# Kernel tuning notes

Measured on AMD Instinct MI355X. Metric: run time of the kernel, lower is better.

The kernel has to match this reference:

```python
import jax, jax.numpy as jnp
import numpy as np

NUM_SIN = 8
HIDDEN = 64
COND = 128
OUT = 4
SQRT2 = 1.4142135623730951


def coords_to_sinusoidals(coords):
    # coords: [..., 2]; per-frequency blocks of 4: [sin_x, sin_y, cos_x, cos_y]
    freqs = 2.0 ** jnp.arange(NUM_SIN, dtype=coords.dtype)  # mult freq_type, multiplier=2
    ang = coords[..., None, :] * freqs[:, None]              # [..., 8, 2]
    emb = jnp.concatenate([jnp.sin(ang), jnp.cos(ang)], axis=-1)  # [..., 8, 4]
    return emb.reshape(coords.shape[:-1] + (2 * 2 * NUM_SIN,))


def equal_linear(x, w, b, lrelu):
    scale = 1.0 / np.sqrt(w.shape[1])  # lr_mul = 1
    y = x @ (w * scale).T + b
    if lrelu:
        y = jax.nn.leaky_relu(y, 0.2) * SQRT2  # fused_lrelu
    return y


def setup_inputs() -> dict:
    key = jax.random.key(0)
    ks = jax.random.split(key, 8)
    coords = jax.random.normal(ks[0], (8, 256, 256, 2), dtype=jnp.float32)
    c = jax.random.normal(ks[1], (8, COND), dtype=jnp.float32)
    freq_unlock = jax.random.uniform(ks[2], (1,), dtype=jnp.float32)
    in1 = 2 * 2 * NUM_SIN + COND  # 160
    in2 = HIDDEN + COND           # 192
    w1 = jax.random.normal(ks[3], (HIDDEN, in1), dtype=jnp.float32)
    w2 = jax.random.normal(ks[4], (HIDDEN, in2), dtype=jnp.float32)
    w3 = jax.random.normal(ks[5], (HIDDEN, in2), dtype=jnp.float32)
    w4 = jax.random.normal(ks[6], (OUT, in2), dtype=jnp.float32)
    b1 = jnp.zeros((HIDDEN,), jnp.float32)
    b2 = jnp.zeros((HIDDEN,), jnp.float32)
    b3 = jnp.zeros((HIDDEN,), jnp.float32)
    b4 = jnp.zeros((OUT,), jnp.float32)
    return {"coords": coords, "c": c, "freq_unlock": freq_unlock,
            "w1": w1, "b1": b1, "w2": w2, "b2": b2,
            "w3": w3, "b3": b3, "w4": w4, "b4": b4}


def reference(coords, c, freq_unlock, w1, b1, w2, b2, w3, b3, w4, b4):
    B, H, W, _ = coords.shape
    emb = coords_to_sinusoidals(coords / 10.0)  # [B,H,W,32]
    # progressive frequency masking
    limits = jnp.arange(1, NUM_SIN + 1, dtype=coords.dtype) / (NUM_SIN + 1)
    weights = jnp.clip((freq_unlock[0] - limits) * (NUM_SIN + 1), 0.0, 1.0)  # [8]
    emb = emb * jnp.repeat(weights, 4)  # blocks of 4 per frequency
    x = emb.reshape(B * H * W, -1)
    cf = jnp.broadcast_to(c[:, None, None, :], (B, H, W, COND)).reshape(B * H * W, COND)
    h = equal_linear(jnp.concatenate([x, cf], -1), w1, b1, True)
    h = equal_linear(jnp.concatenate([h, cf], -1), w2, b2, True)
    h = equal_linear(jnp.concatenate([h, cf], -1), w3, b3, True)
    h = equal_linear(jnp.concatenate([h, cf], -1), w4, b4, False)
    out = h.reshape(B, H, W, OUT)
    # radius masking
    radius = jnp.sqrt(jnp.sum(coords ** 2, axis=-1, keepdims=True))
    out = out * (1.0 - jnp.tanh(jax.nn.relu(radius - 1.0)))
    return out
```

## Files before the change

kernel.cpp:

```cpp
#include <hip/hip_runtime.h>
#include <math.h>


typedef _Float16 half2v __attribute__((ext_vector_type(2)));
typedef __fp16   fp16x2 __attribute__((ext_vector_type(2)));
typedef _Float16 half4v __attribute__((ext_vector_type(4)));
typedef _Float16 half8  __attribute__((ext_vector_type(8)));
typedef float f32x16 __attribute__((ext_vector_type(16)));

#define SCALE1 0.0790569415042094833f
#define SCALE2 0.0721687836487032206f
#define SQRT2F 1.41421356237309515f

#define FE_L1 0
#define FE_L2 256
#define FE_L3 768
#define FE_L4 1280
#define FE_TOT 1536
#define OFF_CB1 6144
#define OFF_CB2 6656
#define OFF_CB3 7168
#define OFF_CB4 7680

__global__ __launch_bounds__(256) void prep_kernel(
    const float* __restrict__ c, const float* __restrict__ fu,
    const float* __restrict__ w1, const float* __restrict__ b1,
    const float* __restrict__ w2, const float* __restrict__ b2,
    const float* __restrict__ w3, const float* __restrict__ b3,
    const float* __restrict__ w4, const float* __restrict__ b4,
    float* __restrict__ ws)
{
  int t = blockIdx.x * 256 + threadIdx.x;
  if (t < 12288) {
    _Float16* fr = (_Float16*)ws;
    int e, Ktm;
    const float* w; float scale; int stride; bool perm;
    if (t < 2048)       { e = t;         Ktm = 2; w = w1; scale = SCALE1;          stride = 160; perm = false; }
    else if (t < 6144)  { e = t - 2048;  Ktm = 4; w = w2; scale = SCALE2 * SQRT2F; stride = 192; perm = true;  }
    else if (t < 10240) { e = t - 6144;  Ktm = 4; w = w3; scale = SCALE2 * SQRT2F; stride = 192; perm = true;  }
    else                { e = t - 10240; Ktm = 4; w = w4; scale = SCALE2 * SQRT2F; stride = 192; perm = true;  }
    int til  = e >> 9;
    int lane = (e >> 3) & 63;
    int r    = e & 7;
    int q    = lane >> 5;
    int mt = til / Ktm, kt = til - mt * Ktm;
    int j = 32 * mt + (lane & 31);
    int k;
    if (perm) {
      k = 32 * (kt >> 1) + 16 * (kt & 1) + 8 * (r >> 2) + 4 * q + (r & 3);
    } else {
      k = 16 * kt + 8 * q + r;
    }
    float val;
    if (t < 2048) {
      float mw = (fu[0] - (float)((k >> 2) + 1) * (1.0f / 9.0f)) * 9.0f;
      mw = fminf(fmaxf(mw, 0.0f), 1.0f);
      val = w[j * stride + k] * scale * mw;
    } else if (t >= 10240) {
      val = (j < 4) ? w[j * stride + k] * scale : 0.0f;
    } else {
      val = w[j * stride + k] * scale;
    }
    fr[t] = (_Float16)val;
  } else if (t < 12288 + 2048) {
    int u = t - 12288;
    int grp = u >> 9;
    const float* wr; float bias; float scale; int outoff;
    int b, j;
    if (grp < 3) {
      b = (u & 511) >> 6; j = u & 63;
      if (grp == 0)      { wr = w1 + j * 160 + 32; bias = b1[j]; scale = SCALE1; outoff = OFF_CB1 + b * 64 + j; }
      else if (grp == 1) { wr = w2 + j * 192 + 64; bias = b2[j]; scale = SCALE2; outoff = OFF_CB2 + b * 64 + j; }
      else               { wr = w3 + j * 192 + 64; bias = b3[j]; scale = SCALE2; outoff = OFF_CB3 + b * 64 + j; }
    } else {
      int u2 = u - 1536;
      if (u2 >= 32) return;
      b = u2 >> 2; j = u2 & 3;
      wr = w4 + j * 192 + 64; bias = b4[j]; scale = SCALE2; outoff = OFF_CB4 + b * 4 + j;
    }
    const float4* wv = (const float4*)wr;
    const float4* cv = (const float4*)(c + b * 128);
    float4 s = make_float4(0.f, 0.f, 0.f, 0.f);
    #pragma unroll
    for (int k = 0; k < 32; ++k) {
      float4 a = wv[k], d = cv[k];
      s.x = fmaf(a.x, d.x, s.x);
      s.y = fmaf(a.y, d.y, s.y);
      s.z = fmaf(a.z, d.z, s.z);
      s.w = fmaf(a.w, d.w, s.w);
    }
    float dot = (s.x + s.y) + (s.z + s.w);
    ws[outoff] = fmaf(scale, dot, bias);
  }
}

__global__ __launch_bounds__(256, 4) void decoder_main(
    const float2* __restrict__ coords, const float* __restrict__ ws,
    float4* __restrict__ out)
{
  __shared__ __align__(16) _Float16 sfr_raw[FE_TOT * 8];
  half8* __restrict__ sfr = (half8*)sfr_raw;

  const int tid  = threadIdx.x;
  const int lane = tid & 63;
  const int wave = tid >> 6;
  const int base = blockIdx.x * 256 + wave * 64;
  const int b    = base >> 16;
  const int col  = lane & 31;
  const bool hi  = lane >= 32;
  const int q4   = hi ? 4 : 0;

  const half8* __restrict__ gfr = (const half8*)ws;
  #pragma unroll
  for (int i = 0; i < 6; ++i) {
    const int e = tid + 256 * i;
    sfr[e] = gfr[e];
  }

  const float* __restrict__ cb1 = ws + OFF_CB1 + b * 64;
  const float* __restrict__ cb2 = ws + OFF_CB2 + b * 64;
  const float* __restrict__ cb3 = ws + OFF_CB3 + b * 64;
  const float* __restrict__ cb4 = ws + OFF_CB4 + b * 4;

  const int p0 = base + col, p1 = base + 32 + col;
  const float2 cc0 = coords[p0];
  const float2 cc1 = coords[p1];

  half8 bf[2][2];
  {
    const float qm = hi ? 0.4f : 0.1f;
    auto chain = [](float a, float* s, float* c) {
      float s0 = __sinf(a), c0 = __cosf(a);
      s[0] = s0; c[0] = c0;
      float s1 = 2.f * s0 * c0, c1 = (c0 - s0) * (c0 + s0);
      s[1] = s1; c[1] = c1;
      float s2 = 2.f * s1 * c1, c2 = (c1 - s1) * (c1 + s1);
      float s3 = 2.f * s2 * c2, c3 = (c2 - s2) * (c2 + s2);
      float s4 = 2.f * s3 * c3, c4 = (c3 - s3) * (c3 + s3);
      s[2] = s4; c[2] = c4;
      float s5 = 2.f * s4 * c4, c5 = (c4 - s4) * (c4 + s4);
      s[3] = s5; c[3] = c5;
    };
    #pragma unroll
    for (int nt = 0; nt < 2; ++nt) {
      const float2 cc = nt ? cc1 : cc0;
      float sx[4], cx[4], sy[4], cy[4];
      chain(cc.x * qm, sx, cx);
      chain(cc.y * qm, sy, cy);
      #pragma unroll
      for (int kt = 0; kt < 2; ++kt) {
        const int i0 = 2 * kt, i1 = 2 * kt + 1;
        half2v p0v = __builtin_bit_cast(half2v, __builtin_amdgcn_cvt_pkrtz(sx[i0], sy[i0]));
        half2v p1v = __builtin_bit_cast(half2v, __builtin_amdgcn_cvt_pkrtz(cx[i0], cy[i0]));
        half2v p2v = __builtin_bit_cast(half2v, __builtin_amdgcn_cvt_pkrtz(sx[i1], sy[i1]));
        half2v p3v = __builtin_bit_cast(half2v, __builtin_amdgcn_cvt_pkrtz(cx[i1], cy[i1]));
        half4v q0 = __builtin_shufflevector(p0v, p1v, 0, 1, 2, 3);
        half4v q1 = __builtin_shufflevector(p2v, p3v, 0, 1, 2, 3);
        bf[nt][kt] = __builtin_shufflevector(q0, q1, 0, 1, 2, 3, 4, 5, 6, 7);
      }
    }
  }

  __syncthreads();

  f32x16 acc[2][2];
  half8 nbf[2][4];

  auto transition = [&]() {
    #pragma unroll
    for (int mt = 0; mt < 2; ++mt)
      #pragma unroll
      for (int nt = 0; nt < 2; ++nt) {
        #pragma unroll
        for (int h = 0; h < 2; ++h) {
          half2v pp[4];
          #pragma unroll
          for (int p = 0; p < 4; ++p) {
            fp16x2 t = __builtin_amdgcn_cvt_pkrtz(acc[mt][nt][8 * h + 2 * p],
                                                  acc[mt][nt][8 * h + 2 * p + 1]);
            pp[p] = __builtin_bit_cast(half2v, t);
          }
          half4v q0 = __builtin_shufflevector(pp[0], pp[1], 0, 1, 2, 3);
          half4v q1 = __builtin_shufflevector(pp[2], pp[3], 0, 1, 2, 3);
          half8 f = __builtin_shufflevector(q0, q1, 0, 1, 2, 3, 4, 5, 6, 7);
          half8 f2 = f * (_Float16)0.2f;
          nbf[nt][2 * mt + h] = __builtin_elementwise_max(f, f2);
        }
      }
  };

  auto init_acc = [&](const float* __restrict__ cb) {
    #pragma unroll
    for (int mt = 0; mt < 2; ++mt)
      #pragma unroll
      for (int g = 0; g < 4; ++g) {
        const float4 f = *(const float4*)(cb + 32 * mt + 8 * g + q4);
        #pragma unroll
        for (int nt = 0; nt < 2; ++nt) {
          acc[mt][nt][4 * g + 0] = f.x;
          acc[mt][nt][4 * g + 1] = f.y;
          acc[mt][nt][4 * g + 2] = f.z;
          acc[mt][nt][4 * g + 3] = f.w;
        }
      }
  };

  init_acc(cb1);
  #pragma unroll
  for (int kt = 0; kt < 2; ++kt) {
    half8 a0 = sfr[FE_L1 + (0 * 2 + kt) * 64 + lane];
    half8 a1 = sfr[FE_L1 + (1 * 2 + kt) * 64 + lane];
    acc[0][0] = __builtin_amdgcn_mfma_f32_32x32x16_f16(a0, bf[0][kt], acc[0][0], 0, 0, 0);
    acc[0][1] = __builtin_amdgcn_mfma_f32_32x32x16_f16(a0, bf[1][kt], acc[0][1], 0, 0, 0);
    acc[1][0] = __builtin_amdgcn_mfma_f32_32x32x16_f16(a1, bf[0][kt], acc[1][0], 0, 0, 0);
    acc[1][1] = __builtin_amdgcn_mfma_f32_32x32x16_f16(a1, bf[1][kt], acc[1][1], 0, 0, 0);
  }
  transition();

  #pragma unroll
  for (int layer = 0; layer < 2; ++layer) {
    const int fe = layer == 0 ? FE_L2 : FE_L3;
    init_acc(layer == 0 ? cb2 : cb3);
    #pragma unroll
    for (int kt = 0; kt < 4; ++kt) {
      half8 a0 = sfr[fe + (0 * 4 + kt) * 64 + lane];
      half8 a1 = sfr[fe + (1 * 4 + kt) * 64 + lane];
      acc[0][0] = __builtin_amdgcn_mfma_f32_32x32x16_f16(a0, nbf[0][kt], acc[0][0], 0, 0, 0);
      acc[0][1] = __builtin_amdgcn_mfma_f32_32x32x16_f16(a0, nbf[1][kt], acc[0][1], 0, 0, 0);
      acc[1][0] = __builtin_amdgcn_mfma_f32_32x32x16_f16(a1, nbf[0][kt], acc[1][0], 0, 0, 0);
      acc[1][1] = __builtin_amdgcn_mfma_f32_32x32x16_f16(a1, nbf[1][kt], acc[1][1], 0, 0, 0);
    }
    transition();
  }

  f32x16 acc4[2];
  {
    const float c0 = cb4[0], c1 = cb4[1], c2 = cb4[2], c3 = cb4[3];
    #pragma unroll
    for (int r = 0; r < 16; ++r) { acc4[0][r] = 0.f; acc4[1][r] = 0.f; }
    if (!hi) {
      acc4[0][0] = c0; acc4[0][1] = c1; acc4[0][2] = c2; acc4[0][3] = c3;
      acc4[1][0] = c0; acc4[1][1] = c1; acc4[1][2] = c2; acc4[1][3] = c3;
    }
  }
  #pragma unroll
  for (int kt = 0; kt < 4; ++kt) {
    half8 a0 = sfr[FE_L4 + kt * 64 + lane];
    acc4[0] = __builtin_amdgcn_mfma_f32_32x32x16_f16(a0, nbf[0][kt], acc4[0], 0, 0, 0);
    acc4[1] = __builtin_amdgcn_mfma_f32_32x32x16_f16(a0, nbf[1][kt], acc4[1], 0, 0, 0);
  }

  if (!hi) {
    #pragma unroll
    for (int nt = 0; nt < 2; ++nt) {
      const float2 cc = nt ? cc1 : cc0;
      const float rad = sqrtf(cc.x * cc.x + cc.y * cc.y);
      const float tt = fmaxf(rad - 1.0f, 0.0f);
      const float m = 2.0f / (__expf(2.0f * tt) + 1.0f);
      out[nt ? p1 : p0] = make_float4(acc4[nt][0] * m, acc4[nt][1] * m,
                                      acc4[nt][2] * m, acc4[nt][3] * m);
    }
  }
}

extern "C" void kernel_launch(void* const* d_in, const int* in_sizes, int n_in,
                              void* d_out, int out_size, void* d_ws, size_t ws_size,
                              hipStream_t stream) {
  const float* coords = (const float*)d_in[0];
  const float* c      = (const float*)d_in[1];
  const float* fu     = (const float*)d_in[2];
  const float* w1     = (const float*)d_in[3];
  const float* b1     = (const float*)d_in[4];
  const float* w2     = (const float*)d_in[5];
  const float* b2     = (const float*)d_in[6];
  const float* w3     = (const float*)d_in[7];
  const float* b3     = (const float*)d_in[8];
  const float* w4     = (const float*)d_in[9];
  const float* b4     = (const float*)d_in[10];
  float* ws  = (float*)d_ws;
  float* out = (float*)d_out;

  int npix = in_sizes[0] / 2;

  prep_kernel<<<56, 256, 0, stream>>>(c, fu, w1, b1, w2, b2, w3, b3, w4, b4, ws);
  decoder_main<<<npix / 256, 256, 0, stream>>>(
      (const float2*)coords, ws, (float4*)out);
}
```

Baseline: 97.80 us.

## Process two pixel tiles per block and stage weights via direct global-to-LDS loads

Each block now handles 512 pixels in two sequential passes, so the 24KB fp16 weight fragment load into LDS is amortized over twice the work and only one barrier is needed. Weights and per-batch bias vectors are loaded with global_load_lds (bypassing VGPRs), and biases now come from LDS instead of global memory. Halving the grid reduces the number of blocks and may reduce parallelism or tail balance, and the wave-3-only bias load relies on the single barrier for visibility.

```diff
diff --git a/kernel.cpp b/kernel.cpp
--- a/kernel.cpp
+++ b/kernel.cpp
@@ -99,13 +99,13 @@
     float4* __restrict__ out)
 {
   __shared__ __align__(16) _Float16 sfr_raw[FE_TOT * 8];
+  __shared__ __align__(16) float scb[256];
   half8* __restrict__ sfr = (half8*)sfr_raw;
 
   const int tid  = threadIdx.x;
   const int lane = tid & 63;
   const int wave = tid >> 6;
-  const int base = blockIdx.x * 256 + wave * 64;
-  const int b    = base >> 16;
+  const int b    = blockIdx.x >> 7;
   const int col  = lane & 31;
   const bool hi  = lane >= 32;
   const int q4   = hi ? 4 : 0;
@@ -113,55 +113,31 @@
   const half8* __restrict__ gfr = (const half8*)ws;
   #pragma unroll
   for (int i = 0; i < 6; ++i) {
-    const int e = tid + 256 * i;
-    sfr[e] = gfr[e];
+    const int e0 = wave * 64 + 256 * i;
+    __builtin_amdgcn_global_load_lds(
+        (const __attribute__((address_space(1))) void*)(gfr + e0 + lane),
+        (__attribute__((address_space(3))) void*)(sfr_raw + e0 * 8),
+        16, 0, 0);
   }
-
-  const float* __restrict__ cb1 = ws + OFF_CB1 + b * 64;
-  const float* __restrict__ cb2 = ws + OFF_CB2 + b * 64;
-  const float* __restrict__ cb3 = ws + OFF_CB3 + b * 64;
-  const float* __restrict__ cb4 = ws + OFF_CB4 + b * 4;
-
-  const int p0 = base + col, p1 = base + 32 + col;
-  const float2 cc0 = coords[p0];
-  const float2 cc1 = coords[p1];
-
-  half8 bf[2][2];
-  {
-    const float qm = hi ? 0.4f : 0.1f;
-    auto chain = [](float a, float* s, float* c) {
-      float s0 = __sinf(a), c0 = __cosf(a);
-      s[0] = s0; c[0] = c0;
-      float s1 = 2.f * s0 * c0, c1 = (c0 - s0) * (c0 + s0);
-      s[1] = s1; c[1] = c1;
-      float s2 = 2.f * s1 * c1, c2 = (c1 - s1) * (c1 + s1);
-      float s3 = 2.f * s2 * c2, c3 = (c2 - s2) * (c2 + s2);
-      float s4 = 2.f * s3 * c3, c4 = (c3 - s3) * (c3 + s3);
-      s[2] = s4; c[2] = c4;
-      float s5 = 2.f * s4 * c4, c5 = (c4 - s4) * (c4 + s4);
-      s[3] = s5; c[3] = c5;
-    };
-    #pragma unroll
-    for (int nt = 0; nt < 2; ++nt) {
-      const float2 cc = nt ? cc1 : cc0;
-      float sx[4], cx[4], sy[4], cy[4];
-      chain(cc.x * qm, sx, cx);
-      chain(cc.y * qm, sy, cy);
-      #pragma unroll
-      for (int kt = 0; kt < 2; ++kt) {
-        const int i0 = 2 * kt, i1 = 2 * kt + 1;
-        half2v p0v = __builtin_bit_cast(half2v, __builtin_amdgcn_cvt_pkrtz(sx[i0], sy[i0]));
-        half2v p1v = __builtin_bit_cast(half2v, __builtin_amdgcn_cvt_pkrtz(cx[i0], cy[i0]));
-        half2v p2v = __builtin_bit_cast(half2v, __builtin_amdgcn_cvt_pkrtz(sx[i1], sy[i1]));
-        half2v p3v = __builtin_bit_cast(half2v, __builtin_amdgcn_cvt_pkrtz(cx[i1], cy[i1]));
-        half4v q0 = __builtin_shufflevector(p0v, p1v, 0, 1, 2, 3);
-        half4v q1 = __builtin_shufflevector(p2v, p3v, 0, 1, 2, 3);
-        bf[nt][kt] = __builtin_shufflevector(q0, q1, 0, 1, 2, 3, 4, 5, 6, 7);
-      }
-    }
+  if (wave == 3) {
+    __builtin_amdgcn_global_load_lds(
+        (const __attribute__((address_space(1))) void*)(ws + OFF_CB1 + b * 64 + lane),
+        (__attribute__((address_space(3))) void*)(scb + 0), 4, 0, 0);
+    __builtin_amdgcn_global_load_lds(
+        (const __attribute__((address_space(1))) void*)(ws + OFF_CB2 + b * 64 + lane),
+        (__attribute__((address_space(3))) void*)(scb + 64), 4, 0, 0);
+    __builtin_amdgcn_global_load_lds(
+        (const __attribute__((address_space(1))) void*)(ws + OFF_CB3 + b * 64 + lane),
+        (__attribute__((address_space(3))) void*)(scb + 128), 4, 0, 0);
+    __builtin_amdgcn_global_load_lds(
+        (const __attribute__((address_space(1))) void*)(ws + OFF_CB4 + b * 4 + lane),
+        (__attribute__((address_space(3))) void*)(scb + 192), 4, 0, 0);
   }
 
-  __syncthreads();
+  const float2* __restrict__ cptr = coords + blockIdx.x * 512 + wave * 64;
+  float2 cc[2][2];
+  cc[0][0] = cptr[col];       cc[0][1] = cptr[32 + col];
+  cc[1][0] = cptr[256 + col]; cc[1][1] = cptr[288 + col];
 
   f32x16 acc[2][2];
   half8 nbf[2][4];
@@ -205,60 +181,101 @@
       }
   };
 
-  init_acc(cb1);
   #pragma unroll
-  for (int kt = 0; kt < 2; ++kt) {
-    half8 a0 = sfr[FE_L1 + (0 * 2 + kt) * 64 + lane];
-    half8 a1 = sfr[FE_L1 + (1 * 2 + kt) * 64 + lane];
-    acc[0][0] = __builtin_amdgcn_mfma_f32_32x32x16_f16(a0, bf[0][kt], acc[0][0], 0, 0, 0);
-    acc[0][1] = __builtin_amdgcn_mfma_f32_32x32x16_f16(a0, bf[1][kt], acc[0][1], 0, 0, 0);
-    acc[1][0] = __builtin_amdgcn_mfma_f32_32x32x16_f16(a1, bf[0][kt], acc[1][0], 0, 0, 0);
-    acc[1][1] = __builtin_amdgcn_mfma_f32_32x32x16_f16(a1, bf[1][kt], acc[1][1], 0, 0, 0);
-  }
-  transition();
-
-  #pragma unroll
-  for (int layer = 0; layer < 2; ++layer) {
-    const int fe = layer == 0 ? FE_L2 : FE_L3;
-    init_acc(layer == 0 ? cb2 : cb3);
+  for (int t = 0; t < 2; ++t) {
+    half8 bf[2][2];
+    {
+      const float qm = hi ? 0.4f : 0.1f;
+      auto chain = [](float a, float* s, float* c) {
+        float s0 = __sinf(a), c0 = __cosf(a);
+        s[0] = s0; c[0] = c0;
+        float s1 = 2.f * s0 * c0, c1 = (c0 - s0) * (c0 + s0);
+        s[1] = s1; c[1] = c1;
+        float s2 = 2.f * s1 * c1, c2 = (c1 - s1) * (c1 + s1);
+        float s3 = 2.f * s2 * c2, c3 = (c2 - s2) * (c2 + s2);
+        float s4 = 2.f * s3 * c3, c4 = (c3 - s3) * (c3 + s3);
+        s[2] = s4; c[2] = c4;
+        float s5 = 2.f * s4 * c4, c5 = (c4 - s4) * (c4 + s4);
+        s[3] = s5; c[3] = c5;
+      };
+      #pragma unroll
+      for (int nt = 0; nt < 2; ++nt) {
+        const float2 ccv = cc[t][nt];
+        float sx[4], cx[4], sy[4], cy[4];
+        chain(ccv.x * qm, sx, cx);
+        chain(ccv.y * qm, sy, cy);
+        #pragma unroll
+        for (int kt = 0; kt < 2; ++kt) {
+          const int i0 = 2 * kt, i1 = 2 * kt + 1;
+          half2v p0v = __builtin_bit_cast(half2v, __builtin_amdgcn_cvt_pkrtz(sx[i0], sy[i0]));
+          half2v p1v = __builtin_bit_cast(half2v, __builtin_amdgcn_cvt_pkrtz(cx[i0], cy[i0]));
+          half2v p2v = __builtin_bit_cast(half2v, __builtin_amdgcn_cvt_pkrtz(sx[i1], sy[i1]));
+          half2v p3v = __builtin_bit_cast(half2v, __builtin_amdgcn_cvt_pkrtz(cx[i1], cy[i1]));
+          half4v q0 = __builtin_shufflevector(p0v, p1v, 0, 1, 2, 3);
+          half4v q1 = __builtin_shufflevector(p2v, p3v, 0, 1, 2, 3);
+          bf[nt][kt] = __builtin_shufflevector(q0, q1, 0, 1, 2, 3, 4, 5, 6, 7);
+        }
+      }
+    }
+
+    if (t == 0) __syncthreads();
+
+    init_acc(scb + 0);
+    #pragma unroll
+    for (int kt = 0; kt < 2; ++kt) {
+      half8 a0 = sfr[FE_L1 + (0 * 2 + kt) * 64 + lane];
+      half8 a1 = sfr[FE_L1 + (1 * 2 + kt) * 64 + lane];
+      acc[0][0] = __builtin_amdgcn_mfma_f32_32x32x16_f16(a0, bf[0][kt], acc[0][0], 0, 0, 0);
+      acc[0][1] = __builtin_amdgcn_mfma_f32_32x32x16_f16(a0, bf[1][kt], acc[0][1], 0, 0, 0);
+      acc[1][0] = __builtin_amdgcn_mfma_f32_32x32x16_f16(a1, bf[0][kt], acc[1][0], 0, 0, 0);
+      acc[1][1] = __builtin_amdgcn_mfma_f32_32x32x16_f16(a1, bf[1][kt], acc[1][1], 0, 0, 0);
+    }
+    transition();
+
+    #pragma unroll
+    for (int layer = 0; layer < 2; ++layer) {
+      const int fe = layer == 0 ? FE_L2 : FE_L3;
+      init_acc(layer == 0 ? scb + 64 : scb + 128);
+      #pragma unroll
+      for (int kt = 0; kt < 4; ++kt) {
+        half8 a0 = sfr[fe + (0 * 4 + kt) * 64 + lane];
+        half8 a1 = sfr[fe + (1 * 4 + kt) * 64 + lane];
+        acc[0][0] = __builtin_amdgcn_mfma_f32_32x32x16_f16(a0, nbf[0][kt], acc[0][0], 0, 0, 0);
+        acc[0][1] = __builtin_amdgcn_mfma_f32_32x32x16_f16(a0, nbf[1][kt], acc[0][1], 0, 0, 0);
+        acc[1][0] = __builtin_amdgcn_mfma_f32_32x32x16_f16(a1, nbf[0][kt], acc[1][0], 0, 0, 0);
+        acc[1][1] = __builtin_amdgcn_mfma_f32_32x32x16_f16(a1, nbf[1][kt], acc[1][1], 0, 0, 0);
+      }
+      transition();
+    }
+
+    f32x16 acc4[2];
+    {
+      const float c0 = scb[192], c1 = scb[193], c2 = scb[194], c3 = scb[195];
+      #pragma unroll
+      for (int r = 0; r < 16; ++r) { acc4[0][r] = 0.f; acc4[1][r] = 0.f; }
+      if (!hi) {
+        acc4[0][0] = c0; acc4[0][1] = c1; acc4[0][2] = c2; acc4[0][3] = c3;
+        acc4[1][0] = c0; acc4[1][1] = c1; acc4[1][2] = c2; acc4[1][3] = c3;
+      }
+    }
     #pragma unroll
     for (int kt = 0; kt < 4; ++kt) {
-      half8 a0 = sfr[fe + (0 * 4 + kt) * 64 + lane];
-      half8 a1 = sfr[fe + (1 * 4 + kt) * 64 + lane];
-      acc[0][0] = __builtin_amdgcn_mfma_f32_32x32x16_f16(a0, nbf[0][kt], acc[0][0], 0, 0, 0);
-      acc[0][1] = __builtin_amdgcn_mfma_f32_32x32x16_f16(a0, nbf[1][kt], acc[0][1], 0, 0, 0);
-      acc[1][0] = __builtin_amdgcn_mfma_f32_32x32x16_f16(a1, nbf[0][kt], acc[1][0], 0, 0, 0);
-      acc[1][1] = __builtin_amdgcn_mfma_f32_32x32x16_f16(a1, nbf[1][kt], acc[1][1], 0, 0, 0);
-    }
-    transition();
-  }
-
-  f32x16 acc4[2];
-  {
-    const float c0 = cb4[0], c1 = cb4[1], c2 = cb4[2], c3 = cb4[3];
-    #pragma unroll
-    for (int r = 0; r < 16; ++r) { acc4[0][r] = 0.f; acc4[1][r] = 0.f; }
+      half8 a0 = sfr[FE_L4 + kt * 64 + lane];
+      acc4[0] = __builtin_amdgcn_mfma_f32_32x32x16_f16(a0, nbf[0][kt], acc4[0], 0, 0, 0);
+      acc4[1] = __builtin_amdgcn_mfma_f32_32x32x16_f16(a0, nbf[1][kt], acc4[1], 0, 0, 0);
+    }
+
     if (!hi) {
-      acc4[0][0] = c0; acc4[0][1] = c1; acc4[0][2] = c2; acc4[0][3] = c3;
-      acc4[1][0] = c0; acc4[1][1] = c1; acc4[1][2] = c2; acc4[1][3] = c3;
-    }
-  }
-  #pragma unroll
-  for (int kt = 0; kt < 4; ++kt) {
-    half8 a0 = sfr[FE_L4 + kt * 64 + lane];
-    acc4[0] = __builtin_amdgcn_mfma_f32_32x32x16_f16(a0, nbf[0][kt], acc4[0], 0, 0, 0);
-    acc4[1] = __builtin_amdgcn_mfma_f32_32x32x16_f16(a0, nbf[1][kt], acc4[1], 0, 0, 0);
-  }
-
-  if (!hi) {
-    #pragma unroll
-    for (int nt = 0; nt < 2; ++nt) {
-      const float2 cc = nt ? cc1 : cc0;
-      const float rad = sqrtf(cc.x * cc.x + cc.y * cc.y);
-      const float tt = fmaxf(rad - 1.0f, 0.0f);
-      const float m = 2.0f / (__expf(2.0f * tt) + 1.0f);
-      out[nt ? p1 : p0] = make_float4(acc4[nt][0] * m, acc4[nt][1] * m,
-                                      acc4[nt][2] * m, acc4[nt][3] * m);
+      const int pbase = blockIdx.x * 512 + t * 256 + wave * 64 + col;
+      #pragma unroll
+      for (int nt = 0; nt < 2; ++nt) {
+        const float2 ccv = cc[t][nt];
+        const float rad = sqrtf(ccv.x * ccv.x + ccv.y * ccv.y);
+        const float tt = fmaxf(rad - 1.0f, 0.0f);
+        const float m = 2.0f / (__expf(2.0f * tt) + 1.0f);
+        out[pbase + 32 * nt] = make_float4(acc4[nt][0] * m, acc4[nt][1] * m,
+                                           acc4[nt][2] * m, acc4[nt][3] * m);
+      }
     }
   }
 }
@@ -283,6 +300,6 @@
   int npix = in_sizes[0] / 2;
 
   prep_kernel<<<56, 256, 0, stream>>>(c, fu, w1, b1, w2, b2, w3, b3, w4, b4, ws);
-  decoder_main<<<npix / 256, 256, 0, stream>>>(
+  decoder_main<<<npix / 512, 256, 0, stream>>>(
       (const float2*)coords, ws, (float4*)out);
 }
```

After: 95.67 us. -2.2%, faster.
